# Kernel tuning notes

Measured on AMD Instinct MI355X. Metric: run time of the kernel, lower is better.

Reference implementation:

```python
import jax, jax.numpy as jnp
import numpy as np

N = 100000   # nodes
DEG = 16     # in-degree per node
E = N * DEG  # edges
D = 64       # embedding_dim


def mobius_addition(x, y, c):
    xy = jnp.sum(x * y, axis=-1, keepdims=True)
    x2 = jnp.sum(x * x, axis=-1, keepdims=True)
    y2 = jnp.sum(y * y, axis=-1, keepdims=True)
    num = (1 + 2 * c * xy + c * y2) * x + (1 - c * x2) * y
    den = 1 + 2 * c * xy + c * c * x2 * y2
    return num / den


def exp_map(x, v, c):
    vn = jnp.linalg.norm(v, axis=-1, keepdims=True)
    sc = jnp.sqrt(c)
    second = jnp.tanh(sc * vn / 2) * v / (sc * vn)
    return mobius_addition(x, second, c)


def log_map(x, y, c):
    add = mobius_addition(-x, y, c)
    an = jnp.linalg.norm(add, axis=-1, keepdims=True)
    sc = jnp.sqrt(c)
    return 2 / sc * jnp.arctanh(sc * an) * add / an


def setup_inputs() -> dict:
    key = jax.random.key(0)
    ks = jax.random.split(key, 6)
    # scale so points are well inside the Poincare ball (atanh domain)
    x = jax.random.normal(ks[0], (N, D), jnp.float32) * 0.01
    src = jax.random.randint(ks[1], (E,), 0, N, dtype=jnp.int32)
    # every node gets exactly DEG in-edges -> no isolated nodes (avoids 0/0 in exp_map)
    dst = jnp.repeat(jnp.arange(N, dtype=jnp.int32), DEG)
    s = 1.0 / np.sqrt(D)
    Wq = jax.random.normal(ks[2], (D, D), jnp.float32) * s
    Wk = jax.random.normal(ks[3], (D, D), jnp.float32) * s
    Wv = jax.random.normal(ks[4], (D, D), jnp.float32) * s
    bq = jnp.zeros((D,), jnp.float32)
    bk = jnp.zeros((D,), jnp.float32)
    bv = jnp.zeros((D,), jnp.float32)
    curvature = jnp.ones((1,), jnp.float32)
    return {"x": x, "curvature": curvature, "Wq": Wq, "bq": bq, "Wk": Wk,
            "bk": bk, "Wv": Wv, "bv": bv, "src": src, "dst": dst}


def reference(x, curvature, Wq, bq, Wk, bk, Wv, bv, src, dst):
    c = curvature  # (1,), broadcasts against (N,1) keepdim norms
    n = x.shape[0]
    origin = jnp.zeros_like(x[:1])  # (1, D)
    tangent = log_map(origin, x, c)  # (N, D)
    # torch nn.Linear: y = x @ W.T + b
    q = tangent @ Wq.T + bq
    k = tangent @ Wk.T + bk
    v = tangent @ Wv.T + bv
    scale = jnp.asarray(x.shape[-1] ** 0.5, x.dtype)
    # per-edge score: <k[src], q[dst]> / sqrt(d)
    scores = jnp.einsum('ed,ed->e', k[src], q[dst]) / scale  # (E,)
    # segment (per-dst) softmax over incoming edges
    smax = jax.ops.segment_max(scores, dst, num_segments=n)
    ex = jnp.exp(scores - smax[dst])
    ssum = jax.ops.segment_sum(ex, dst, num_segments=n)
    alpha = ex / ssum[dst]  # (E,)
    # weighted scatter-sum of src values
    h = jax.ops.segment_sum(alpha[:, None] * v[src], dst, num_segments=n)  # (N, D)
    return exp_map(origin, h, c)
```

## Files before the change

kernel.cpp:

```cpp
#include <hip/hip_runtime.h>
#include <hip/hip_bf16.h>
#include <math.h>


typedef __attribute__((ext_vector_type(8))) short bf16x8;
typedef __attribute__((ext_vector_type(4))) float f32x4;

static __device__ __forceinline__ short f2bf(float f) {
    union { __hip_bfloat16 h; short s; } u; u.h = __float2bfloat16(f); return u.s;
}
static __device__ __forceinline__ float bflo(unsigned u) {
    return __uint_as_float(u << 16);
}
static __device__ __forceinline__ float bfhi(unsigned u) {
    return __uint_as_float(u & 0xffff0000u);
}

#define TSTRIDE 72

__global__ __launch_bounds__(256) void qkv_kernel(
    const float* __restrict__ x,
    const float* __restrict__ cur,
    const float* __restrict__ Wq, const float* __restrict__ bq,
    const float* __restrict__ Wk, const float* __restrict__ bk,
    const float* __restrict__ Wv, const float* __restrict__ bv,
    float* __restrict__ q, __hip_bfloat16* __restrict__ kv, int N)
{
    __shared__ short tL[128 * TSTRIDE];
    const int tid = threadIdx.x;
    const int w = tid >> 6, lane = tid & 63;
    const int blockBase = blockIdx.x * 128;
    const float sc = sqrtf(cur[0]);

    const int rr = lane >> 2, p = lane & 3;
    #pragma unroll
    for (int it = 0; it < 2; ++it) {
        const int rloc = w * 32 + it * 16 + rr;
        int row = blockBase + rloc; if (row >= N) row = N - 1;
        const float4* xr = (const float4*)(x + (size_t)row * 64 + p * 16);
        float4 x0 = xr[0], x1 = xr[1], x2 = xr[2], x3 = xr[3];
        float pn = x0.x*x0.x + x0.y*x0.y + x0.z*x0.z + x0.w*x0.w
                 + x1.x*x1.x + x1.y*x1.y + x1.z*x1.z + x1.w*x1.w
                 + x2.x*x2.x + x2.y*x2.y + x2.z*x2.z + x2.w*x2.w
                 + x3.x*x3.x + x3.y*x3.y + x3.z*x3.z + x3.w*x3.w;
        pn += __shfl_xor(pn, 1, 64);
        pn += __shfl_xor(pn, 2, 64);
        float z = sc * sqrtf(pn);
        float ts = (z > 1e-12f) ? (__logf((1.0f + z) / (1.0f - z)) / z) : 2.0f;
        bf16x8 t0, t1;
        t0[0]=f2bf(ts*x0.x); t0[1]=f2bf(ts*x0.y); t0[2]=f2bf(ts*x0.z); t0[3]=f2bf(ts*x0.w);
        t0[4]=f2bf(ts*x1.x); t0[5]=f2bf(ts*x1.y); t0[6]=f2bf(ts*x1.z); t0[7]=f2bf(ts*x1.w);
        t1[0]=f2bf(ts*x2.x); t1[1]=f2bf(ts*x2.y); t1[2]=f2bf(ts*x2.z); t1[3]=f2bf(ts*x2.w);
        t1[4]=f2bf(ts*x3.x); t1[5]=f2bf(ts*x3.y); t1[6]=f2bf(ts*x3.z); t1[7]=f2bf(ts*x3.w);
        bf16x8* dst = (bf16x8*)&tL[rloc * TSTRIDE + p * 16];
        dst[0] = t0; dst[1] = t1;
    }
    __syncthreads();

    const int n16 = lane & 15, quad = lane >> 4;
    bf16x8 Bf[3][2];
    float bias[3];
    int matv[3], col0v[3];
    #pragma unroll
    for (int tt = 0; tt < 3; ++tt) {
        const int tile = w * 3 + tt;
        const int mat = tile >> 2;
        const int col0 = (tile & 3) * 16;
        matv[tt] = mat; col0v[tt] = col0;
        const float* Wm = (mat == 0) ? Wq : (mat == 1) ? Wk : Wv;
        const float* bm = (mat == 0) ? bq : (mat == 1) ? bk : bv;
        const float* srcp = Wm + (col0 + n16) * 64 + quad * 8;
        #pragma unroll
        for (int h = 0; h < 2; ++h) {
            float4 a = *(const float4*)(srcp + h * 32);
            float4 b = *(const float4*)(srcp + h * 32 + 4);
            bf16x8 f;
            f[0]=f2bf(a.x); f[1]=f2bf(a.y); f[2]=f2bf(a.z); f[3]=f2bf(a.w);
            f[4]=f2bf(b.x); f[5]=f2bf(b.y); f[6]=f2bf(b.z); f[7]=f2bf(b.w);
            Bf[tt][h] = f;
        }
        bias[tt] = bm[col0 + n16];
    }

    for (int nt = 0; nt < 8; ++nt) {
        const short* ar = &tL[(nt * 16 + n16) * TSTRIDE + quad * 8];
        bf16x8 A0 = *(const bf16x8*)ar;
        bf16x8 A1 = *(const bf16x8*)(ar + 32);
        #pragma unroll
        for (int tt = 0; tt < 3; ++tt) {
            f32x4 acc = { bias[tt], bias[tt], bias[tt], bias[tt] };
            acc = __builtin_amdgcn_mfma_f32_16x16x32_bf16(A0, Bf[tt][0], acc, 0, 0, 0);
            acc = __builtin_amdgcn_mfma_f32_16x16x32_bf16(A1, Bf[tt][1], acc, 0, 0, 0);
            const int mat = matv[tt], col0 = col0v[tt];
            #pragma unroll
            for (int r4 = 0; r4 < 4; ++r4) {
                const int node = blockBase + nt * 16 + quad * 4 + r4;
                if (node < N) {
                    if (mat == 0) {
                        q[(size_t)node * 64 + col0 + n16] = acc[r4];
                    } else {
                        kv[(size_t)node * 128 + (mat == 2 ? 64 : 0) + col0 + n16]
                            = __float2bfloat16(acc[r4]);
                    }
                }
            }
        }
    }
}

__global__ __launch_bounds__(256) void attn_kernel(
    const float* __restrict__ q, const __hip_bfloat16* __restrict__ kv,
    const int* __restrict__ src, const float* __restrict__ cur,
    float* __restrict__ out, int N)
{
    __shared__ float s_alpha[4][16];
    __shared__ int   s_src[4][16];
    const int tid = threadIdx.x;
    const int w = tid >> 6, lane = tid & 63;
    int node = blockIdx.x * 4 + w;
    if (node >= N) node = N - 1;

    const int j = lane >> 2, p = lane & 3;
    const int sj = src[node * 16 + j];
    if (p == 0) s_src[w][j] = sj;

    const uint4*  kr = (const uint4*)(kv + (size_t)sj * 128) + p * 2;
    const float4* qr = (const float4*)(q + (size_t)node * 64) + p * 4;
    uint4 a = kr[0], b = kr[1];
    float4 q0 = qr[0], q1 = qr[1], q2 = qr[2], q3 = qr[3];
    float acc = 0.f;
    acc += bflo(a.x) * q0.x + bfhi(a.x) * q0.y;
    acc += bflo(a.y) * q0.z + bfhi(a.y) * q0.w;
    acc += bflo(a.z) * q1.x + bfhi(a.z) * q1.y;
    acc += bflo(a.w) * q1.z + bfhi(a.w) * q1.w;
    acc += bflo(b.x) * q2.x + bfhi(b.x) * q2.y;
    acc += bflo(b.y) * q2.z + bfhi(b.y) * q2.w;
    acc += bflo(b.z) * q3.x + bfhi(b.z) * q3.y;
    acc += bflo(b.w) * q3.z + bfhi(b.w) * q3.w;
    acc += __shfl_xor(acc, 1, 64);
    acc += __shfl_xor(acc, 2, 64);
    float score = acc * 0.125f;

    float mx = score;
    #pragma unroll
    for (int m = 4; m < 64; m <<= 1) mx = fmaxf(mx, __shfl_xor(mx, m, 64));
    float ex = __expf(score - mx);
    float ssum = ex;
    #pragma unroll
    for (int m = 4; m < 64; m <<= 1) ssum += __shfl_xor(ssum, m, 64);
    if (p == 0) s_alpha[w][j] = ex / ssum;
    __syncthreads();

    float h = 0.f;
    #pragma unroll
    for (int jj = 0; jj < 16; ++jj) {
        unsigned raw = *(const unsigned short*)(kv + (size_t)s_src[w][jj] * 128 + 64 + lane);
        h = fmaf(s_alpha[w][jj], bflo(raw), h);
    }

    float n2 = h * h;
    #pragma unroll
    for (int m = 1; m < 64; m <<= 1) n2 += __shfl_xor(n2, m, 64);
    const float sc = sqrtf(cur[0]);
    float z = sc * sqrtf(n2);
    float scale = (z > 1e-12f) ? (tanhf(0.5f * z) / z) : 0.5f;
    out[(size_t)node * 64 + lane] = scale * h;
}

extern "C" void kernel_launch(void* const* d_in, const int* in_sizes, int n_in,
                              void* d_out, int out_size, void* d_ws, size_t ws_size,
                              hipStream_t stream)
{
    const float* x   = (const float*)d_in[0];
    const float* cur = (const float*)d_in[1];
    const float* Wq  = (const float*)d_in[2];
    const float* bq  = (const float*)d_in[3];
    const float* Wk  = (const float*)d_in[4];
    const float* bk  = (const float*)d_in[5];
    const float* Wv  = (const float*)d_in[6];
    const float* bv  = (const float*)d_in[7];
    const int* src = (const int*)d_in[8];

    const int N = in_sizes[0] / 64;

    float* q = (float*)d_ws;
    __hip_bfloat16* kv = (__hip_bfloat16*)(q + (size_t)N * 64);

    const int blocks1 = (N + 127) / 128;
    const int blocks2 = (N + 3) / 4;
    qkv_kernel<<<blocks1, 256, 0, stream>>>(x, cur, Wq, bq, Wk, bk, Wv, bv,
                                            q, kv, N);
    attn_kernel<<<blocks2, 256, 0, stream>>>(q, kv, src, cur,
                                             (float*)d_out, N);
}
```

Before: 165.5 us.

## Store Q as bf16 and K as fp8, split V buffer, vectorize V gather

Q is now stored as bf16 instead of fp32 and K as fp8 (e4m3) instead of bf16, and V moves into its own contiguous bf16 buffer. This cuts the bytes written by the projection kernel and read by the random per-edge gathers in the attention kernel. The V aggregation now has each half-wave handle 8 edges with 32-bit loads of two channels, combined with one cross-half shuffle, and tanh is rewritten via expf. Dropping K to fp8 reduces score accuracy and may push error closer to the tolerance.

Result: no change. 163.0 us (-1.5%).

```diff
diff --git a/kernel.cpp b/kernel.cpp
--- a/kernel.cpp
+++ b/kernel.cpp
@@ -5,6 +5,7 @@
 
 typedef __attribute__((ext_vector_type(8))) short bf16x8;
 typedef __attribute__((ext_vector_type(4))) float f32x4;
+typedef __attribute__((ext_vector_type(2))) float f32x2;
 
 static __device__ __forceinline__ short f2bf(float f) {
     union { __hip_bfloat16 h; short s; } u; u.h = __float2bfloat16(f); return u.s;
@@ -24,7 +25,8 @@
     const float* __restrict__ Wq, const float* __restrict__ bq,
     const float* __restrict__ Wk, const float* __restrict__ bk,
     const float* __restrict__ Wv, const float* __restrict__ bv,
-    float* __restrict__ q, __hip_bfloat16* __restrict__ kv, int N)
+    unsigned short* __restrict__ qb, unsigned char* __restrict__ kf8,
+    unsigned short* __restrict__ vb, int N)
 {
     __shared__ short tL[128 * TSTRIDE];
     const int tid = threadIdx.x;
@@ -96,11 +98,14 @@
             for (int r4 = 0; r4 < 4; ++r4) {
                 const int node = blockBase + nt * 16 + quad * 4 + r4;
                 if (node < N) {
+                    const int o = node * 64 + col0 + n16;
                     if (mat == 0) {
-                        q[(size_t)node * 64 + col0 + n16] = acc[r4];
+                        qb[o] = (unsigned short)f2bf(acc[r4]);
+                    } else if (mat == 1) {
+                        int pk = __builtin_amdgcn_cvt_pk_fp8_f32(acc[r4], acc[r4], 0, false);
+                        kf8[o] = (unsigned char)(pk & 0xff);
                     } else {
-                        kv[(size_t)node * 128 + (mat == 2 ? 64 : 0) + col0 + n16]
-                            = __float2bfloat16(acc[r4]);
+                        vb[o] = (unsigned short)f2bf(acc[r4]);
                     }
                 }
             }
@@ -109,8 +114,9 @@
 }
 
 __global__ __launch_bounds__(256) void attn_kernel(
-    const float* __restrict__ q, const __hip_bfloat16* __restrict__ kv,
-    const int* __restrict__ src, const float* __restrict__ cur,
+    const unsigned short* __restrict__ qb, const unsigned char* __restrict__ kf8,
+    const unsigned short* __restrict__ vb, const int* __restrict__ src,
+    const float* __restrict__ cur,
     float* __restrict__ out, int N)
 {
     __shared__ float s_alpha[4][16];
@@ -124,19 +130,21 @@
     const int sj = src[node * 16 + j];
     if (p == 0) s_src[w][j] = sj;
 
-    const uint4*  kr = (const uint4*)(kv + (size_t)sj * 128) + p * 2;
-    const float4* qr = (const float4*)(q + (size_t)node * 64) + p * 4;
-    uint4 a = kr[0], b = kr[1];
-    float4 q0 = qr[0], q1 = qr[1], q2 = qr[2], q3 = qr[3];
+    uint4 kd = *(const uint4*)(kf8 + sj * 64 + p * 16);
+    const uint4* qp = (const uint4*)(qb + node * 64 + p * 16);
+    uint4 qa = qp[0], qc = qp[1];
+    unsigned kws[4] = { kd.x, kd.y, kd.z, kd.w };
+    unsigned qws[8] = { qa.x, qa.y, qa.z, qa.w, qc.x, qc.y, qc.z, qc.w };
     float acc = 0.f;
-    acc += bflo(a.x) * q0.x + bfhi(a.x) * q0.y;
-    acc += bflo(a.y) * q0.z + bfhi(a.y) * q0.w;
-    acc += bflo(a.z) * q1.x + bfhi(a.z) * q1.y;
-    acc += bflo(a.w) * q1.z + bfhi(a.w) * q1.w;
-    acc += bflo(b.x) * q2.x + bfhi(b.x) * q2.y;
-    acc += bflo(b.y) * q2.z + bfhi(b.y) * q2.w;
-    acc += bflo(b.z) * q3.x + bfhi(b.z) * q3.y;
-    acc += bflo(b.w) * q3.z + bfhi(b.w) * q3.w;
+    #pragma unroll
+    for (int gw = 0; gw < 4; ++gw) {
+        f32x2 k0 = __builtin_amdgcn_cvt_pk_f32_fp8(kws[gw], false);
+        f32x2 k1 = __builtin_amdgcn_cvt_pk_f32_fp8(kws[gw], true);
+        acc = fmaf(k0[0], bflo(qws[2 * gw]), acc);
+        acc = fmaf(k0[1], bfhi(qws[2 * gw]), acc);
+        acc = fmaf(k1[0], bflo(qws[2 * gw + 1]), acc);
+        acc = fmaf(k1[1], bfhi(qws[2 * gw + 1]), acc);
+    }
     acc += __shfl_xor(acc, 1, 64);
     acc += __shfl_xor(acc, 2, 64);
     float score = acc * 0.125f;
@@ -151,20 +159,40 @@
     if (p == 0) s_alpha[w][j] = ex / ssum;
     __syncthreads();
 
-    float h = 0.f;
-    #pragma unroll
-    for (int jj = 0; jj < 16; ++jj) {
-        unsigned raw = *(const unsigned short*)(kv + (size_t)s_src[w][jj] * 128 + 64 + lane);
-        h = fmaf(s_alpha[w][jj], bflo(raw), h);
-    }
-
-    float n2 = h * h;
-    #pragma unroll
-    for (int m = 1; m < 64; m <<= 1) n2 += __shfl_xor(n2, m, 64);
+    const int half = lane >> 5, l5 = lane & 31;
+    int   srcv[8];
+    float alphav[8];
+    {
+        const uint4* sp = (const uint4*)&s_src[w][half * 8];
+        const f32x4* ap = (const f32x4*)&s_alpha[w][half * 8];
+        uint4 s0 = sp[0], s1 = sp[1];
+        f32x4 a0 = ap[0], a1 = ap[1];
+        srcv[0]=s0.x; srcv[1]=s0.y; srcv[2]=s0.z; srcv[3]=s0.w;
+        srcv[4]=s1.x; srcv[5]=s1.y; srcv[6]=s1.z; srcv[7]=s1.w;
+        alphav[0]=a0[0]; alphav[1]=a0[1]; alphav[2]=a0[2]; alphav[3]=a0[3];
+        alphav[4]=a1[0]; alphav[5]=a1[1]; alphav[6]=a1[2]; alphav[7]=a1[3];
+    }
+    float hx = 0.f, hy = 0.f;
+    #pragma unroll
+    for (int i = 0; i < 8; ++i) {
+        unsigned u = *(const unsigned*)(vb + (srcv[i] << 6) + (l5 << 1));
+        hx = fmaf(alphav[i], bflo(u), hx);
+        hy = fmaf(alphav[i], bfhi(u), hy);
+    }
+    hx += __shfl_xor(hx, 32, 64);
+    hy += __shfl_xor(hy, 32, 64);
+
+    float n2 = hx * hx + hy * hy;
+    #pragma unroll
+    for (int m = 1; m < 32; m <<= 1) n2 += __shfl_xor(n2, m, 64);
     const float sc = sqrtf(cur[0]);
     float z = sc * sqrtf(n2);
-    float scale = (z > 1e-12f) ? (tanhf(0.5f * z) / z) : 0.5f;
-    out[(size_t)node * 64 + lane] = scale * h;
+    float e = __expf(z);
+    float scale = (z > 1e-12f) ? ((e - 1.0f) / (z * (e + 1.0f))) : 0.5f;
+    if (half == 0) {
+        float2 o2 = make_float2(scale * hx, scale * hy);
+        *(float2*)(out + (size_t)node * 64 + (l5 << 1)) = o2;
+    }
 }
 
 extern "C" void kernel_launch(void* const* d_in, const int* in_sizes, int n_in,
@@ -183,13 +211,14 @@
 
     const int N = in_sizes[0] / 64;
 
-    float* q = (float*)d_ws;
-    __hip_bfloat16* kv = (__hip_bfloat16*)(q + (size_t)N * 64);
+    unsigned short* qb = (unsigned short*)d_ws;
+    unsigned char*  kf8 = (unsigned char*)(qb + (size_t)N * 64);
+    unsigned short* vb = (unsigned short*)(kf8 + (size_t)N * 64);
 
     const int blocks1 = (N + 127) / 128;
     const int blocks2 = (N + 3) / 4;
     qkv_kernel<<<blocks1, 256, 0, stream>>>(x, cur, Wq, bq, Wk, bk, Wv, bv,
-                                            q, kv, N);
-    attn_kernel<<<blocks2, 256, 0, stream>>>(q, kv, src, cur,
+                                            qb, kf8, vb, N);
+    attn_kernel<<<blocks2, 256, 0, stream>>>(qb, kf8, vb, src, cur,
                                              (float*)d_out, N);
 }
```
